# Performance work log

Hardware: AMD Instinct MI355X
Metric: run time of the kernel (lower is better)

Reference implementation:

```python
import jax, jax.numpy as jnp
import numpy as np

N, E, G = 50000, 800000, 64
IN, EDGE = 128, 16
HID, H = 32, 4
FHID, HF = 64, 4
OUT = 16
NEG_SLOPE = 0.2


def _segment_softmax(logits, seg, num):
    m = jax.ops.segment_max(logits, seg, num_segments=num)
    m = jnp.where(jnp.isfinite(m), m, 0.0)
    p = jnp.exp(logits - m[seg])
    s = jax.ops.segment_sum(p, seg, num_segments=num)
    return p / (s[seg] + 1e-16)


def gatv2(x, src, dst, eattr, Wl, bl, Wr, br, We, att, bias, concat):
    # PyG GATv2Conv with add_self_loops=True (edge_attr fill_value='mean')
    n = x.shape[0]
    heads, ch = att.shape
    ones = jnp.ones((src.shape[0],), x.dtype)
    cnt = jax.ops.segment_sum(ones, dst, num_segments=n)
    mean_attr = jax.ops.segment_sum(eattr, dst, num_segments=n) / jnp.maximum(cnt, 1.0)[:, None]
    loop = jnp.arange(n)
    s = jnp.concatenate([src, loop])
    d = jnp.concatenate([dst, loop])
    ea = jnp.concatenate([eattr, mean_attr], axis=0)
    xl = (x @ Wl + bl).reshape(n, heads, ch)   # lin_l (source)
    xr = (x @ Wr + br).reshape(n, heads, ch)   # lin_r (target)
    ee = (ea @ We).reshape(-1, heads, ch)      # lin_edge (no bias)
    z = jax.nn.leaky_relu(xl[s] + xr[d] + ee, NEG_SLOPE)  # [E+N, H, C]
    logits = jnp.einsum('ehc,hc->eh', z, att)
    alpha = _segment_softmax(logits, d, n)
    out = jax.ops.segment_sum(alpha[:, :, None] * xl[s], d, num_segments=n)  # [N, H, C]
    out = out.reshape(n, heads * ch) if concat else out.mean(axis=1)
    return out + bias


def _forward(x, edge_attr, src, dst, batch,
             Wl0, bl0, Wr0, br0, We0, att0, bo0,
             Wlh, blh, Wrh, brh, Weh, atth, boh,
             Wlf, blf, Wrf, brf, Wef, attf, bof,
             Wlin, blin):
    h1 = jax.nn.relu(gatv2(x, src, dst, edge_attr, Wl0, bl0, Wr0, br0, We0, att0, bo0, True))
    h2 = jax.nn.relu(gatv2(h1, src, dst, edge_attr, Wlh, blh, Wrh, brh, Weh, atth, boh, True))
    h3 = jax.nn.relu(gatv2(h2, src, dst, edge_attr, Wlf, blf, Wrf, brf, Wef, attf, bof, False))
    # global_mean_pool over graphs
    gsum = jax.ops.segment_sum(h3, batch, num_segments=G)
    gcnt = jax.ops.segment_sum(jnp.ones((h3.shape[0],), h3.dtype), batch, num_segments=G)
    g = gsum / jnp.maximum(gcnt, 1.0)[:, None]
    return g @ Wlin + blin  # final_dropout inactive in eval mode


def setup_inputs():
    key = jax.random.key(0)
    ks = jax.random.split(key, 20)
    def p(i, shape, fan_in):
        return jax.random.normal(ks[i], shape, jnp.float32) / np.sqrt(fan_in)
    z = lambda *s: jnp.zeros(s, jnp.float32)
    return {
        'x': jax.random.normal(ks[0], (N, IN), jnp.float32),
        'edge_index': jax.random.randint(ks[1], (2, E), 0, N),
        'batch': jnp.sort(jax.random.randint(ks[2], (N,), 0, G)),
        'edge_attr': jax.random.normal(ks[3], (E, EDGE), jnp.float32),
        'Wl0': p(4, (IN, H * HID), IN), 'bl0': z(H * HID),
        'Wr0': p(5, (IN, H * HID), IN), 'br0': z(H * HID),
        'We0': p(6, (EDGE, H * HID), EDGE), 'att0': p(7, (H, HID), HID), 'bo0': z(H * HID),
        'Wlh': p(8, (H * HID, H * HID), H * HID), 'blh': z(H * HID),
        'Wrh': p(9, (H * HID, H * HID), H * HID), 'brh': z(H * HID),
        'Weh': p(10, (EDGE, H * HID), EDGE), 'atth': p(11, (H, HID), HID), 'boh': z(H * HID),
        'Wlf': p(12, (H * HID, HF * FHID), H * HID), 'blf': z(HF * FHID),
        'Wrf': p(13, (H * HID, HF * FHID), H * HID), 'brf': z(HF * FHID),
        'Wef': p(14, (EDGE, HF * FHID), EDGE), 'attf': p(15, (HF, FHID), FHID), 'bof': z(FHID),
        'Wlin': p(16, (FHID, OUT), FHID), 'blin': z(OUT),
    }


def reference(x, edge_index, batch, edge_attr, Wl0, bl0, Wr0, br0, We0, att0, bo0, Wlh, blh, Wrh, brh, Weh, atth, boh, Wlf, blf, Wrf, brf, Wef, attf, bof, Wlin, blin):
    return _forward(x, edge_attr, edge_index[0], edge_index[1], batch,
                    Wl0, bl0, Wr0, br0, We0, att0, bo0,
                    Wlh, blh, Wrh, brh, Weh, atth, boh,
                    Wlf, blf, Wrf, brf, Wef, attf, bof,
                    Wlin, blin)
```

## Files before the change

### kernel.cpp

```cpp
#include <hip/hip_runtime.h>
#include <cstddef>

#define NSLOPE 0.2f

constexpr int NN = 50000;
constexpr int EE = 800000;
constexpr int GG = 64;
constexpr int SCAN_B = 1024;

typedef unsigned short ushort_t;
typedef unsigned int uint_t;
typedef __bf16 bhalf;
typedef bhalf bhalf8 __attribute__((ext_vector_type(8)));
typedef float floatx4 __attribute__((ext_vector_type(4)));
typedef _Float16 half_t;
typedef half_t half2_t __attribute__((ext_vector_type(2)));

__device__ __forceinline__ ushort_t f2b(float f) {
  unsigned int u = __float_as_uint(f);
  unsigned int r = (u + 0x7fffu + ((u >> 16) & 1u)) >> 16;
  return (ushort_t)r;
}
__device__ __forceinline__ float b2f(ushort_t b) {
  return __uint_as_float(((unsigned int)b) << 16);
}
__device__ __forceinline__ uint_t packh2(float a, float b) {
  half2_t h = {(half_t)a, (half_t)b};
  return __builtin_bit_cast(uint_t, h);
}
__device__ __forceinline__ float dot2acc(uint_t ea, half2_t w, float c) {
  half2_t a = __builtin_bit_cast(half2_t, ea);
#if __has_builtin(__builtin_amdgcn_fdot2)
  return __builtin_amdgcn_fdot2(a, w, c, false);
#else
  return c + (float)a.x * (float)w.x + (float)a.y * (float)w.y;
#endif
}
__device__ __forceinline__ float fexp2(float x) {
#if __has_builtin(__builtin_amdgcn_exp2f)
  return __builtin_amdgcn_exp2f(x);
#else
  return exp2f(x);
#endif
}

__device__ __forceinline__ float red16(float x) {
  int v = __builtin_bit_cast(int, x);
  x += __builtin_bit_cast(float, __builtin_amdgcn_update_dpp(0, v, 0xB1, 0xF, 0xF, true));
  v = __builtin_bit_cast(int, x);
  x += __builtin_bit_cast(float, __builtin_amdgcn_update_dpp(0, v, 0x4E, 0xF, 0xF, true));
  v = __builtin_bit_cast(int, x);
  x += __builtin_bit_cast(float, __builtin_amdgcn_update_dpp(0, v, 0x124, 0xF, 0xF, true));
  v = __builtin_bit_cast(int, x);
  x += __builtin_bit_cast(float, __builtin_amdgcn_update_dpp(0, v, 0x128, 0xF, 0xF, true));
  return x;
}

__global__ void hist_kernel(const int* __restrict__ dst, int* __restrict__ hist, int E) {
  int e = blockIdx.x * blockDim.x + threadIdx.x;
  if (e < E) atomicAdd(&hist[dst[e]], 1);
}

__global__ void scan_block_kernel(const int* __restrict__ in, int* __restrict__ out,
                                  int* __restrict__ bsum, int n) {
  __shared__ int tmp[SCAN_B];
  int gid = blockIdx.x * SCAN_B + threadIdx.x;
  int v = (gid < n) ? in[gid] : 0;
  tmp[threadIdx.x] = v;
  __syncthreads();
  for (int off = 1; off < SCAN_B; off <<= 1) {
    int t = (threadIdx.x >= off) ? tmp[threadIdx.x - off] : 0;
    __syncthreads();
    tmp[threadIdx.x] += t;
    __syncthreads();
  }
  if (gid < n) out[gid] = tmp[threadIdx.x];
  if (threadIdx.x == SCAN_B - 1) bsum[blockIdx.x] = tmp[threadIdx.x];
}

__global__ void scan_totals_kernel(const int* __restrict__ bsum, int* __restrict__ boff, int nb) {
  if (blockIdx.x == 0 && threadIdx.x == 0) {
    int run = 0;
    for (int i = 0; i < nb; ++i) { boff[i] = run; run += bsum[i]; }
  }
}

__global__ void add_offsets_kernel(int* __restrict__ rowptr, const int* __restrict__ boff,
                                   int* __restrict__ cursor, int n) {
  int gid = blockIdx.x * SCAN_B + threadIdx.x;
  if (gid == 0) { rowptr[0] = 0; cursor[0] = 0; }
  if (gid < n) {
    int v = rowptr[1 + gid] + boff[blockIdx.x];
    rowptr[1 + gid] = v;
    if (1 + gid < n) cursor[1 + gid] = v;
  }
}

__global__ void scatter_fused_kernel(const int* __restrict__ dst, const int* __restrict__ src,
                                     const float* __restrict__ eattr, int* __restrict__ cursor,
                                     int* __restrict__ srcp, uint_t* __restrict__ eah, int E) {
  int e = blockIdx.x * blockDim.x + threadIdx.x;
  if (e >= E) return;
  const float4* a = reinterpret_cast<const float4*>(eattr + (size_t)e * 16);
  float4 f0 = a[0], f1 = a[1], f2 = a[2], f3 = a[3];
  int pos = atomicAdd(&cursor[dst[e]], 1);
  srcp[pos] = src[e];
  uint4 o0 = make_uint4(packh2(f0.x, f0.y), packh2(f0.z, f0.w),
                        packh2(f1.x, f1.y), packh2(f1.z, f1.w));
  uint4 o1 = make_uint4(packh2(f2.x, f2.y), packh2(f2.z, f2.w),
                        packh2(f3.x, f3.y), packh2(f3.z, f3.w));
  uint4* b = reinterpret_cast<uint4*>(eah + (size_t)pos * 8);
  b[0] = o0; b[1] = o1;
}

__global__ __launch_bounds__(256) void mean_attr_kernel(
    const int* __restrict__ rowptr, const uint_t* __restrict__ eah,
    uint_t* __restrict__ meanattr_h, int N) {
  const int lane = threadIdx.x & 63;
  int d = blockIdx.x * (blockDim.x >> 6) + (threadIdx.x >> 6);
  if (d >= N) return;
  int beg = rowptr[d], end = rowptr[d + 1];
  int k2 = lane & 7;
  int sub = lane >> 3;
  float ax = 0.f, ay = 0.f;
  for (int j = beg + sub; j < end; j += 8) {
    half2_t h = __builtin_bit_cast(half2_t, eah[(size_t)j * 8 + k2]);
    ax += (float)h.x; ay += (float)h.y;
  }
  ax += __shfl_xor(ax, 8);  ay += __shfl_xor(ay, 8);
  ax += __shfl_xor(ax, 16); ay += __shfl_xor(ay, 16);
  ax += __shfl_xor(ax, 32); ay += __shfl_xor(ay, 32);
  if (sub == 0) {
    int c = end - beg; if (c < 1) c = 1;
    float inv = 1.f / (float)c;
    meanattr_h[(size_t)d * 8 + k2] = packh2(ax * inv, ay * inv);
  }
}

__global__ void prep_w_kernel(const float* W0, ushort_t* T0, int n0,
                              const float* W1, ushort_t* T1, int n1,
                              const float* W2, ushort_t* T2, int n2,
                              const float* W3, ushort_t* T3, int n3,
                              const float* W4, ushort_t* T4, int n4,
                              const float* W5, ushort_t* T5, int n5) {
  const float* W; ushort_t* T; int Nc;
  switch (blockIdx.y) {
    case 0: W = W0; T = T0; Nc = n0; break;
    case 1: W = W1; T = T1; Nc = n1; break;
    case 2: W = W2; T = T2; Nc = n2; break;
    case 3: W = W3; T = T3; Nc = n3; break;
    case 4: W = W4; T = T4; Nc = n4; break;
    default: W = W5; T = T5; Nc = n5; break;
  }
  int idx = blockIdx.x * blockDim.x + threadIdx.x;
  if (idx >= Nc * 128) return;
  int n = idx >> 7, k = idx & 127;
  T[idx] = f2b(W[(size_t)k * Nc + n]);
}

__global__ void prep_we_kernel(const float* We0, const float* att0, uint_t* w0, float* a0,
                               const float* We1, const float* att1, uint_t* w1, float* a1,
                               const float* We2, const float* att2, uint_t* w2, float* a2) {
  const float* We; const float* att; uint_t* wp; float* ap; int C;
  switch (blockIdx.y) {
    case 0: We = We0; att = att0; wp = w0; ap = a0; C = 128; break;
    case 1: We = We1; att = att1; wp = w1; ap = a1; C = 128; break;
    default: We = We2; att = att2; wp = w2; ap = a2; C = 256; break;
  }
  int idx = blockIdx.x * blockDim.x + threadIdx.x;
  if (idx >= 9 * C) return;
  if (idx < 8 * C) {
    int sh = (C == 256) ? 8 : 7;
    int k2 = idx >> sh, ch = idx & (C - 1);
    wp[idx] = packh2(We[(size_t)(2 * k2) * C + ch], We[(size_t)(2 * k2 + 1) * C + ch]);
  } else {
    int ch = idx - 8 * C;
    ap[ch] = att[ch] * 1.44269504f;
  }
}

template <typename TA>
__global__ __launch_bounds__(256) void gemm_bt_dual_bf16(
    const TA* __restrict__ Xb,
    const ushort_t* __restrict__ Wt0, const float* __restrict__ b0, ushort_t* __restrict__ Y0,
    const ushort_t* __restrict__ Wt1, const float* __restrict__ b1, ushort_t* __restrict__ Y1,
    int M, int Nc) {
  constexpr int K = 128, BM = 128, LDT = 136;
  __shared__ ushort_t Als[BM * LDT];
  __shared__ ushort_t Bls[BM * LDT];
  int nb = Nc >> 7;
  int half = blockIdx.y / nb;
  int cb = blockIdx.y % nb;
  const ushort_t* Wt = half ? Wt1 : Wt0;
  const float* bias = half ? b1 : b0;
  ushort_t* Y = half ? Y1 : Y0;
  int r0 = blockIdx.x * BM;
  int col0 = cb * 128;
  int tid = threadIdx.x;
  {
    int rl = tid >> 5;
    int kq = (tid & 31) * 4;
#pragma unroll
    for (int s = 0; s < 16; ++s) {
      int row = rl + s * 8;
      int grow = r0 + row;
      ushort4 v = make_ushort4(0, 0, 0, 0);
      if (grow < M) {
        if constexpr (sizeof(TA) == 4) {
          float4 f = *reinterpret_cast<const float4*>(Xb + (size_t)grow * K + kq);
          v = make_ushort4(f2b(f.x), f2b(f.y), f2b(f.z), f2b(f.w));
        } else {
          v = *reinterpret_cast<const ushort4*>(Xb + (size_t)grow * K + kq);
        }
      }
      *reinterpret_cast<ushort4*>(&Als[row * LDT + kq]) = v;
      ushort4 wv = *reinterpret_cast<const ushort4*>(Wt + (size_t)(col0 + row) * K + kq);
      *reinterpret_cast<ushort4*>(&Bls[row * LDT + kq]) = wv;
    }
  }
  __syncthreads();
  int lane = tid & 63;
  int w = tid >> 6;
  int m0 = (w >> 1) * 64;
  int n0 = (w & 1) * 64;
  int rin = lane & 15, quad = lane >> 4;
  floatx4 acc[4][4];
#pragma unroll
  for (int i = 0; i < 4; ++i)
#pragma unroll
    for (int j = 0; j < 4; ++j) acc[i][j] = (floatx4){0.f, 0.f, 0.f, 0.f};
#pragma unroll
  for (int kt = 0; kt < 4; ++kt) {
    int ko = kt * 32 + quad * 8;
    bhalf8 af[4], bf[4];
#pragma unroll
    for (int i = 0; i < 4; ++i)
      af[i] = *reinterpret_cast<const bhalf8*>(&Als[(m0 + i * 16 + rin) * LDT + ko]);
#pragma unroll
    for (int i = 0; i < 4; ++i)
      bf[i] = *reinterpret_cast<const bhalf8*>(&Bls[(n0 + i * 16 + rin) * LDT + ko]);
#pragma unroll
    for (int mi = 0; mi < 4; ++mi)
#pragma unroll
      for (int ni = 0; ni < 4; ++ni)
        acc[mi][ni] = __builtin_amdgcn_mfma_f32_16x16x32_bf16(af[mi], bf[ni], acc[mi][ni], 0, 0, 0);
  }
#pragma unroll
  for (int ni = 0; ni < 4; ++ni) {
    int gcol = col0 + n0 + ni * 16 + rin;
    float bb = bias[gcol];
#pragma unroll
    for (int mi = 0; mi < 4; ++mi) {
      int growb = r0 + m0 + mi * 16 + quad * 4;
#pragma unroll
      for (int r = 0; r < 4; ++r) {
        int grow = growb + r;
        if (grow < M) Y[(size_t)grow * Nc + gcol] = f2b(acc[mi][ni][r] + bb);
      }
    }
  }
}

template <int VPL>
__device__ __forceinline__ void loadb(const ushort_t* p, float* v) {
  if constexpr (VPL == 2) {
    ushort2 t = *reinterpret_cast<const ushort2*>(p);
    v[0] = b2f(t.x); v[1] = b2f(t.y);
  } else {
    ushort4 t = *reinterpret_cast<const ushort4*>(p);
    v[0] = b2f(t.x); v[1] = b2f(t.y); v[2] = b2f(t.z); v[3] = b2f(t.w);
  }
}
template <int VPL>
__device__ __forceinline__ void storeb(ushort_t* p, const float* v) {
  if constexpr (VPL == 2) {
    *reinterpret_cast<ushort2*>(p) = make_ushort2(f2b(v[0]), f2b(v[1]));
  } else {
    *reinterpret_cast<ushort4*>(p) = make_ushort4(f2b(v[0]), f2b(v[1]), f2b(v[2]), f2b(v[3]));
  }
}

template <int VPL>
__device__ __forceinline__ float lrelu_dot(const float* xv, const float* rv,
                                           const half2_t (*wepk)[VPL], const float* areg,
                                           const uint_t* ea) {
  float part = 0.f;
#pragma unroll
  for (int j = 0; j < VPL; ++j) {
    float z = xv[j] + rv[j];
#pragma unroll
    for (int k2 = 0; k2 < 8; ++k2) z = dot2acc(ea[k2], wepk[k2][j], z);
    float zl = fmaxf(z, NSLOPE * z);
    part = fmaf(zl, areg[j], part);
  }
  return red16(part);
}

template <int EB, int VPL, int C>
__device__ __forceinline__ void process_group(
    const int* __restrict__ srcp, const uint_t* __restrict__ eah, int j,
    const ushort_t* __restrict__ xl, int lane, const float* rv,
    const half2_t (*wepk)[VPL], const float* areg,
    float& s, float* acc) {
  int sn[EB];
#pragma unroll
  for (int u = 0; u < EB; ++u) sn[u] = srcp[j + u];
  float xv[EB][VPL];
#pragma unroll
  for (int u = 0; u < EB; ++u) loadb<VPL>(xl + (size_t)sn[u] * C + lane * VPL, xv[u]);
  float lg[EB];
#pragma unroll
  for (int u = 0; u < EB; ++u) {
    const uint4* ap4 = reinterpret_cast<const uint4*>(eah + (size_t)(j + u) * 8);
    uint4 e0 = ap4[0], e1 = ap4[1];
    uint_t ea[8] = {e0.x, e0.y, e0.z, e0.w, e1.x, e1.y, e1.z, e1.w};
    lg[u] = lrelu_dot<VPL>(xv[u], rv, wepk, areg, ea);
  }
  float p[EB], ps = 0.f;
#pragma unroll
  for (int u = 0; u < EB; ++u) { p[u] = fexp2(lg[u]); ps += p[u]; }
  s += ps;
#pragma unroll
  for (int jj = 0; jj < VPL; ++jj) {
    float t = p[0] * xv[0][jj];
#pragma unroll
    for (int u = 1; u < EB; ++u) t = fmaf(p[u], xv[u][jj], t);
    acc[jj] += t;
  }
}

template <int VPL, int C>
__device__ __forceinline__ void process_edge(
    int sn, const uint_t* ea,
    const ushort_t* __restrict__ xl, int lane, const float* rv,
    const half2_t (*wepk)[VPL], const float* areg,
    float& s, float* acc) {
  float xv[VPL];
  loadb<VPL>(xl + (size_t)sn * C + lane * VPL, xv);
  float lg = lrelu_dot<VPL>(xv, rv, wepk, areg, ea);
  float p = fexp2(lg);
  s += p;
#pragma unroll
  for (int jj = 0; jj < VPL; ++jj) acc[jj] = fmaf(p, xv[jj], acc[jj]);
}

template <int C, bool FINAL>
__global__ __launch_bounds__(128) void gat_fused_kernel(
    const int* __restrict__ rowptr,
    const int* __restrict__ srcp, const uint_t* __restrict__ eah,
    const uint_t* __restrict__ meanattr_h,
    const ushort_t* __restrict__ xl, const ushort_t* __restrict__ xr,
    const uint_t* __restrict__ wep,
    const float* __restrict__ atts,
    const float* __restrict__ bias, ushort_t* __restrict__ hout, int N) {
  constexpr int VPL = C / 64;
  const int lane = threadIdx.x & 63;
  int d = __builtin_amdgcn_readfirstlane(blockIdx.x * 2 + (threadIdx.x >> 6));
  if (d >= N) return;

  half2_t wepk[8][VPL];
  float areg[VPL];
#pragma unroll
  for (int k2 = 0; k2 < 8; ++k2)
#pragma unroll
    for (int jj = 0; jj < VPL; ++jj)
      wepk[k2][jj] = __builtin_bit_cast(half2_t, wep[k2 * C + lane * VPL + jj]);
#pragma unroll
  for (int jj = 0; jj < VPL; ++jj) areg[jj] = atts[lane * VPL + jj];

  int beg = rowptr[d], end = rowptr[d + 1];
  float rv[VPL];
  loadb<VPL>(xr + (size_t)d * C + lane * VPL, rv);

  float s = 0.f;
  float acc[VPL];
#pragma unroll
  for (int jj = 0; jj < VPL; ++jj) acc[jj] = 0.f;

  int j = beg;
  if constexpr (C == 128) {
    for (; j + 8 <= end; j += 8)
      process_group<8, VPL, C>(srcp, eah, j, xl, lane, rv, wepk, areg, s, acc);
  }
  for (; j + 4 <= end; j += 4)
    process_group<4, VPL, C>(srcp, eah, j, xl, lane, rv, wepk, areg, s, acc);
  for (; j + 2 <= end; j += 2)
    process_group<2, VPL, C>(srcp, eah, j, xl, lane, rv, wepk, areg, s, acc);
  for (; j < end; ++j)
    process_group<1, VPL, C>(srcp, eah, j, xl, lane, rv, wepk, areg, s, acc);

  {
    const uint4* mp4 = reinterpret_cast<const uint4*>(meanattr_h + (size_t)d * 8);
    uint4 e0 = mp4[0], e1 = mp4[1];
    uint_t ea[8] = {e0.x, e0.y, e0.z, e0.w, e1.x, e1.y, e1.z, e1.w};
    process_edge<VPL, C>(d, ea, xl, lane, rv, wepk, areg, s, acc);
  }

  float inv = 1.f / (s + 1e-16f);
  if constexpr (!FINAL) {
    float res[VPL];
#pragma unroll
    for (int jj = 0; jj < VPL; ++jj) {
      float v = acc[jj] * inv + bias[lane * VPL + jj];
      res[jj] = v > 0.f ? v : 0.f;
    }
    storeb<VPL>(hout + (size_t)d * C + lane * VPL, res);
  } else {
    float v[VPL];
#pragma unroll
    for (int jj = 0; jj < VPL; ++jj) v[jj] = acc[jj] * inv;
#pragma unroll
    for (int jj = 0; jj < VPL; ++jj) {
      v[jj] += __shfl_xor(v[jj], 16);
      v[jj] += __shfl_xor(v[jj], 32);
    }
    if (lane < 16) {
      float res[VPL];
#pragma unroll
      for (int jj = 0; jj < VPL; ++jj) {
        float val = 0.25f * v[jj] + bias[lane * VPL + jj];
        res[jj] = val > 0.f ? val : 0.f;
      }
      storeb<VPL>(hout + (size_t)d * 64 + lane * VPL, res);
    }
  }
}

__global__ __launch_bounds__(256) void pool_kernel(
    const ushort_t* __restrict__ h3, const int* __restrict__ batch,
    float* __restrict__ gsum, float* __restrict__ gcnt, int N) {
  const int lane = threadIdx.x & 63;
  const int w = blockIdx.x * (blockDim.x >> 6) + (threadIdx.x >> 6);
  const int nw = gridDim.x * (blockDim.x >> 6);
  const int chunk = (N + nw - 1) / nw;
  int i0 = w * chunk;
  int i1 = i0 + chunk; if (i1 > N) i1 = N;
  if (i0 >= i1) return;
  int cur = batch[i0];
  float acc = 0.f;
  int cnt = 0;
  for (int i = i0; i < i1; ++i) {
    int g = batch[i];
    if (g != cur) {
      atomicAdd(&gsum[(size_t)cur * 64 + lane], acc);
      if (lane == 0) atomicAdd(&gcnt[cur], (float)cnt);
      acc = 0.f; cnt = 0; cur = g;
    }
    acc += b2f(h3[(size_t)i * 64 + lane]);
    ++cnt;
  }
  atomicAdd(&gsum[(size_t)cur * 64 + lane], acc);
  if (lane == 0) atomicAdd(&gcnt[cur], (float)cnt);
}

__global__ void final_kernel(const float* __restrict__ gsum, const float* __restrict__ gcnt,
                             const float* __restrict__ Wlin, const float* __restrict__ blin,
                             float* __restrict__ out) {
  int idx = blockIdx.x * blockDim.x + threadIdx.x;
  if (idx >= GG * 16) return;
  int g = idx >> 4, o = idx & 15;
  float c = gcnt[g];
  c = c > 1.f ? c : 1.f;
  float inv = 1.f / c;
  float acc = blin[o];
  for (int f = 0; f < 64; ++f) acc = fmaf(gsum[(size_t)g * 64 + f] * inv, Wlin[f * 16 + o], acc);
  out[idx] = acc;
}

extern "C" void kernel_launch(void* const* d_in, const int* in_sizes, int n_in,
                              void* d_out, int out_size, void* d_ws, size_t ws_size,
                              hipStream_t stream) {
  (void)in_sizes; (void)n_in; (void)out_size; (void)ws_size;
  const float* x     = (const float*)d_in[0];
  const int*   eidx  = (const int*)d_in[1];
  const int*   batch = (const int*)d_in[2];
  const float* eattr = (const float*)d_in[3];
  const float* Wl0 = (const float*)d_in[4];  const float* bl0 = (const float*)d_in[5];
  const float* Wr0 = (const float*)d_in[6];  const float* br0 = (const float*)d_in[7];
  const float* We0 = (const float*)d_in[8];  const float* att0 = (const float*)d_in[9];
  const float* bo0 = (const float*)d_in[10];
  const float* Wlh = (const float*)d_in[11]; const float* blh = (const float*)d_in[12];
  const float* Wrh = (const float*)d_in[13]; const float* brh = (const float*)d_in[14];
  const float* Weh = (const float*)d_in[15]; const float* atth = (const float*)d_in[16];
  const float* boh = (const float*)d_in[17];
  const float* Wlf = (const float*)d_in[18]; const float* blf = (const float*)d_in[19];
  const float* Wrf = (const float*)d_in[20]; const float* brf = (const float*)d_in[21];
  const float* Wef = (const float*)d_in[22]; const float* attf = (const float*)d_in[23];
  const float* bof = (const float*)d_in[24];
  const float* Wlin = (const float*)d_in[25]; const float* blin = (const float*)d_in[26];

  const int* src = eidx;
  const int* dst = eidx + EE;

  char* ws = (char*)d_ws;
  size_t off = 0;
  auto take = [&](size_t bytes) -> void* {
    void* p = ws + off;
    off += (bytes + 1023) & ~(size_t)1023;
    return p;
  };
  ushort_t* xl     = (ushort_t*)take((size_t)NN * 256 * 2);
  ushort_t* xr     = (ushort_t*)take((size_t)NN * 256 * 2);
  ushort_t* hb     = (ushort_t*)take((size_t)NN * 128 * 2);
  uint_t* meanattr_h = (uint_t*)take((size_t)NN * 8 * 4);
  int* hist        = (int*)take((size_t)NN * 4);
  float* gsum      = (float*)take((size_t)GG * 64 * 4);
  float* gcnt      = (float*)take((size_t)GG * 4);
  int* rowptr      = (int*)take((size_t)(NN + 1) * 4);
  int* cursor      = (int*)take((size_t)NN * 4);
  int* bsum        = (int*)take(256);
  int* boff        = (int*)take(256);
  ushort_t* wtl0   = (ushort_t*)take((size_t)128 * 128 * 2);
  ushort_t* wtr0   = (ushort_t*)take((size_t)128 * 128 * 2);
  ushort_t* wtlh   = (ushort_t*)take((size_t)128 * 128 * 2);
  ushort_t* wtrh   = (ushort_t*)take((size_t)128 * 128 * 2);
  ushort_t* wtlf   = (ushort_t*)take((size_t)256 * 128 * 2);
  ushort_t* wtrf   = (ushort_t*)take((size_t)256 * 128 * 2);
  int* srcp        = (int*)take((size_t)EE * 4);
  uint_t* eah      = (uint_t*)take((size_t)EE * 8 * 4);
  uint_t* we0p     = (uint_t*)take((size_t)8 * 128 * 4);
  uint_t* wehp     = (uint_t*)take((size_t)8 * 128 * 4);
  uint_t* wefp     = (uint_t*)take((size_t)8 * 256 * 4);
  float* att0s     = (float*)take((size_t)128 * 4);
  float* atths     = (float*)take((size_t)128 * 4);
  float* attfs     = (float*)take((size_t)256 * 4);

  hipMemsetAsync(hist, 0, 200704 + 16384 + 256, stream);
  hist_kernel<<<(EE + 255) / 256, 256, 0, stream>>>(dst, hist, EE);
  int nsb = (NN + SCAN_B - 1) / SCAN_B;
  scan_block_kernel<<<nsb, SCAN_B, 0, stream>>>(hist, rowptr + 1, bsum, NN);
  scan_totals_kernel<<<1, 64, 0, stream>>>(bsum, boff, nsb);
  add_offsets_kernel<<<nsb, SCAN_B, 0, stream>>>(rowptr, boff, cursor, NN);
  scatter_fused_kernel<<<(EE + 255) / 256, 256, 0, stream>>>(dst, src, eattr, cursor, srcp, eah, EE);
  mean_attr_kernel<<<(NN + 3) / 4, 256, 0, stream>>>(rowptr, eah, meanattr_h, NN);
  prep_w_kernel<<<dim3(128, 6), 256, 0, stream>>>(Wl0, wtl0, 128, Wr0, wtr0, 128,
                                                  Wlh, wtlh, 128, Wrh, wtrh, 128,
                                                  Wlf, wtlf, 256, Wrf, wtrf, 256);
  prep_we_kernel<<<dim3(9, 3), 256, 0, stream>>>(We0, att0, we0p, att0s,
                                                 Weh, atth, wehp, atths,
                                                 Wef, attf, wefp, attfs);

  const int GEMM_MB = (NN + 127) / 128;
  const int GAT_BLOCKS = (NN + 1) / 2;

  gemm_bt_dual_bf16<float><<<dim3(GEMM_MB, 2), 256, 0, stream>>>(
      x, wtl0, bl0, xl, wtr0, br0, xr, NN, 128);
  gat_fused_kernel<128, false><<<GAT_BLOCKS, 128, 0, stream>>>(
      rowptr, srcp, eah, meanattr_h, xl, xr, we0p, att0s, bo0, hb, NN);
  gemm_bt_dual_bf16<ushort_t><<<dim3(GEMM_MB, 2), 256, 0, stream>>>(
      hb, wtlh, blh, xl, wtrh, brh, xr, NN, 128);
  gat_fused_kernel<128, false><<<GAT_BLOCKS, 128, 0, stream>>>(
      rowptr, srcp, eah, meanattr_h, xl, xr, wehp, atths, boh, hb, NN);
  gemm_bt_dual_bf16<ushort_t><<<dim3(GEMM_MB, 4), 256, 0, stream>>>(
      hb, wtlf, blf, xl, wtrf, brf, xr, NN, 256);
  gat_fused_kernel<256, true><<<GAT_BLOCKS, 128, 0, stream>>>(
      rowptr, srcp, eah, meanattr_h, xl, xr, wefp, attfs, bof, hb, NN);
  pool_kernel<<<128, 256, 0, stream>>>(hb, batch, gsum, gcnt, NN);
  final_kernel<<<4, 256, 0, stream>>>(gsum, gcnt, Wlin, blin, (float*)d_out);
}
```

Before: 672.7 us.

## Reuse GEMM input tile across both projections, persistent GAT blocks, warp scan

The dual GEMM now loads the A tile once and loops over the left and right weight matrices, so the input is read and converted only once per block instead of once per projection. The GAT kernel becomes a grid-stride persistent kernel with 4096 blocks, so edge weights, attention vectors and bias are loaded once per wave and reused across many nodes instead of reloaded per node. The block-total scan becomes a wavefront shuffle scan instead of a single-thread serial loop. In exchange there are fewer GEMM blocks and a serialized inner loop over the two projections, and the persistent GAT has a static node-to-wave assignment that may load-balance worse on skewed degrees.

```diff
diff --git a/kernel.cpp b/kernel.cpp
--- a/kernel.cpp
+++ b/kernel.cpp
@@ -79,10 +79,14 @@
 }
 
 __global__ void scan_totals_kernel(const int* __restrict__ bsum, int* __restrict__ boff, int nb) {
-  if (blockIdx.x == 0 && threadIdx.x == 0) {
-    int run = 0;
-    for (int i = 0; i < nb; ++i) { boff[i] = run; run += bsum[i]; }
-  }
+  int lane = threadIdx.x;
+  int orig = (lane < nb) ? bsum[lane] : 0;
+  int v = orig;
+  for (int off = 1; off < 64; off <<= 1) {
+    int t = __shfl_up(v, off);
+    if (lane >= off) v += t;
+  }
+  if (lane < nb) boff[lane] = v - orig;
 }
 
 __global__ void add_offsets_kernel(int* __restrict__ rowptr, const int* __restrict__ boff,
@@ -188,74 +192,77 @@
   constexpr int K = 128, BM = 128, LDT = 136;
   __shared__ ushort_t Als[BM * LDT];
   __shared__ ushort_t Bls[BM * LDT];
-  int nb = Nc >> 7;
-  int half = blockIdx.y / nb;
-  int cb = blockIdx.y % nb;
-  const ushort_t* Wt = half ? Wt1 : Wt0;
-  const float* bias = half ? b1 : b0;
-  ushort_t* Y = half ? Y1 : Y0;
   int r0 = blockIdx.x * BM;
-  int col0 = cb * 128;
+  int col0 = blockIdx.y * 128;
   int tid = threadIdx.x;
-  {
-    int rl = tid >> 5;
-    int kq = (tid & 31) * 4;
-#pragma unroll
-    for (int s = 0; s < 16; ++s) {
-      int row = rl + s * 8;
-      int grow = r0 + row;
-      ushort4 v = make_ushort4(0, 0, 0, 0);
-      if (grow < M) {
-        if constexpr (sizeof(TA) == 4) {
-          float4 f = *reinterpret_cast<const float4*>(Xb + (size_t)grow * K + kq);
-          v = make_ushort4(f2b(f.x), f2b(f.y), f2b(f.z), f2b(f.w));
-        } else {
-          v = *reinterpret_cast<const ushort4*>(Xb + (size_t)grow * K + kq);
-        }
+  int rl = tid >> 5;
+  int kq = (tid & 31) * 4;
+#pragma unroll
+  for (int s = 0; s < 16; ++s) {
+    int row = rl + s * 8;
+    int grow = r0 + row;
+    ushort4 v = make_ushort4(0, 0, 0, 0);
+    if (grow < M) {
+      if constexpr (sizeof(TA) == 4) {
+        float4 f = *reinterpret_cast<const float4*>(Xb + (size_t)grow * K + kq);
+        v = make_ushort4(f2b(f.x), f2b(f.y), f2b(f.z), f2b(f.w));
+      } else {
+        v = *reinterpret_cast<const ushort4*>(Xb + (size_t)grow * K + kq);
       }
-      *reinterpret_cast<ushort4*>(&Als[row * LDT + kq]) = v;
-      ushort4 wv = *reinterpret_cast<const ushort4*>(Wt + (size_t)(col0 + row) * K + kq);
-      *reinterpret_cast<ushort4*>(&Bls[row * LDT + kq]) = wv;
-    }
-  }
-  __syncthreads();
+    }
+    *reinterpret_cast<ushort4*>(&Als[row * LDT + kq]) = v;
+  }
   int lane = tid & 63;
   int w = tid >> 6;
   int m0 = (w >> 1) * 64;
   int n0 = (w & 1) * 64;
   int rin = lane & 15, quad = lane >> 4;
-  floatx4 acc[4][4];
-#pragma unroll
-  for (int i = 0; i < 4; ++i)
-#pragma unroll
-    for (int j = 0; j < 4; ++j) acc[i][j] = (floatx4){0.f, 0.f, 0.f, 0.f};
-#pragma unroll
-  for (int kt = 0; kt < 4; ++kt) {
-    int ko = kt * 32 + quad * 8;
-    bhalf8 af[4], bf[4];
+
+  for (int half = 0; half < 2; ++half) {
+    const ushort_t* Wt = half ? Wt1 : Wt0;
+    const float* bias = half ? b1 : b0;
+    ushort_t* Y = half ? Y1 : Y0;
+    __syncthreads();
+#pragma unroll
+    for (int s = 0; s < 16; ++s) {
+      int row = rl + s * 8;
+      ushort4 wv = *reinterpret_cast<const ushort4*>(Wt + (size_t)(col0 + row) * K + kq);
+      *reinterpret_cast<ushort4*>(&Bls[row * LDT + kq]) = wv;
+    }
+    __syncthreads();
+    floatx4 acc[4][4];
 #pragma unroll
     for (int i = 0; i < 4; ++i)
-      af[i] = *reinterpret_cast<const bhalf8*>(&Als[(m0 + i * 16 + rin) * LDT + ko]);
-#pragma unroll
-    for (int i = 0; i < 4; ++i)
-      bf[i] = *reinterpret_cast<const bhalf8*>(&Bls[(n0 + i * 16 + rin) * LDT + ko]);
-#pragma unroll
-    for (int mi = 0; mi < 4; ++mi)
-#pragma unroll
-      for (int ni = 0; ni < 4; ++ni)
-        acc[mi][ni] = __builtin_amdgcn_mfma_f32_16x16x32_bf16(af[mi], bf[ni], acc[mi][ni], 0, 0, 0);
-  }
-#pragma unroll
-  for (int ni = 0; ni < 4; ++ni) {
-    int gcol = col0 + n0 + ni * 16 + rin;
-    float bb = bias[gcol];
-#pragma unroll
-    for (int mi = 0; mi < 4; ++mi) {
-      int growb = r0 + m0 + mi * 16 + quad * 4;
-#pragma unroll
-      for (int r = 0; r < 4; ++r) {
-        int grow = growb + r;
-        if (grow < M) Y[(size_t)grow * Nc + gcol] = f2b(acc[mi][ni][r] + bb);
+#pragma unroll
+      for (int j = 0; j < 4; ++j) acc[i][j] = (floatx4){0.f, 0.f, 0.f, 0.f};
+#pragma unroll
+    for (int kt = 0; kt < 4; ++kt) {
+      int ko = kt * 32 + quad * 8;
+      bhalf8 af[4], bf[4];
+#pragma unroll
+      for (int i = 0; i < 4; ++i)
+        af[i] = *reinterpret_cast<const bhalf8*>(&Als[(m0 + i * 16 + rin) * LDT + ko]);
+#pragma unroll
+      for (int i = 0; i < 4; ++i)
+        bf[i] = *reinterpret_cast<const bhalf8*>(&Bls[(n0 + i * 16 + rin) * LDT + ko]);
+#pragma unroll
+      for (int mi = 0; mi < 4; ++mi)
+#pragma unroll
+        for (int ni = 0; ni < 4; ++ni)
+          acc[mi][ni] = __builtin_amdgcn_mfma_f32_16x16x32_bf16(af[mi], bf[ni], acc[mi][ni], 0, 0, 0);
+    }
+#pragma unroll
+    for (int ni = 0; ni < 4; ++ni) {
+      int gcol = col0 + n0 + ni * 16 + rin;
+      float bb = bias[gcol];
+#pragma unroll
+      for (int mi = 0; mi < 4; ++mi) {
+        int growb = r0 + m0 + mi * 16 + quad * 4;
+#pragma unroll
+        for (int r = 0; r < 4; ++r) {
+          int grow = growb + r;
+          if (grow < M) Y[(size_t)grow * Nc + gcol] = f2b(acc[mi][ni][r] + bb);
+        }
       }
     }
   }
@@ -355,11 +362,11 @@
     const float* __restrict__ bias, ushort_t* __restrict__ hout, int N) {
   constexpr int VPL = C / 64;
   const int lane = threadIdx.x & 63;
-  int d = __builtin_amdgcn_readfirstlane(blockIdx.x * 2 + (threadIdx.x >> 6));
-  if (d >= N) return;
+  const int w0 = blockIdx.x * 2 + (threadIdx.x >> 6);
+  const int nw = gridDim.x * 2;
 
   half2_t wepk[8][VPL];
-  float areg[VPL];
+  float areg[VPL], breg[VPL];
 #pragma unroll
   for (int k2 = 0; k2 < 8; ++k2)
 #pragma unroll
@@ -367,61 +374,67 @@
       wepk[k2][jj] = __builtin_bit_cast(half2_t, wep[k2 * C + lane * VPL + jj]);
 #pragma unroll
   for (int jj = 0; jj < VPL; ++jj) areg[jj] = atts[lane * VPL + jj];
-
-  int beg = rowptr[d], end = rowptr[d + 1];
-  float rv[VPL];
-  loadb<VPL>(xr + (size_t)d * C + lane * VPL, rv);
-
-  float s = 0.f;
-  float acc[VPL];
-#pragma unroll
-  for (int jj = 0; jj < VPL; ++jj) acc[jj] = 0.f;
-
-  int j = beg;
-  if constexpr (C == 128) {
-    for (; j + 8 <= end; j += 8)
-      process_group<8, VPL, C>(srcp, eah, j, xl, lane, rv, wepk, areg, s, acc);
-  }
-  for (; j + 4 <= end; j += 4)
-    process_group<4, VPL, C>(srcp, eah, j, xl, lane, rv, wepk, areg, s, acc);
-  for (; j + 2 <= end; j += 2)
-    process_group<2, VPL, C>(srcp, eah, j, xl, lane, rv, wepk, areg, s, acc);
-  for (; j < end; ++j)
-    process_group<1, VPL, C>(srcp, eah, j, xl, lane, rv, wepk, areg, s, acc);
-
-  {
-    const uint4* mp4 = reinterpret_cast<const uint4*>(meanattr_h + (size_t)d * 8);
-    uint4 e0 = mp4[0], e1 = mp4[1];
-    uint_t ea[8] = {e0.x, e0.y, e0.z, e0.w, e1.x, e1.y, e1.z, e1.w};
-    process_edge<VPL, C>(d, ea, xl, lane, rv, wepk, areg, s, acc);
-  }
-
-  float inv = 1.f / (s + 1e-16f);
-  if constexpr (!FINAL) {
-    float res[VPL];
-#pragma unroll
-    for (int jj = 0; jj < VPL; ++jj) {
-      float v = acc[jj] * inv + bias[lane * VPL + jj];
-      res[jj] = v > 0.f ? v : 0.f;
-    }
-    storeb<VPL>(hout + (size_t)d * C + lane * VPL, res);
-  } else {
-    float v[VPL];
-#pragma unroll
-    for (int jj = 0; jj < VPL; ++jj) v[jj] = acc[jj] * inv;
-#pragma unroll
-    for (int jj = 0; jj < VPL; ++jj) {
-      v[jj] += __shfl_xor(v[jj], 16);
-      v[jj] += __shfl_xor(v[jj], 32);
-    }
-    if (lane < 16) {
+#pragma unroll
+  for (int jj = 0; jj < VPL; ++jj)
+    breg[jj] = (!FINAL || lane < 16) ? bias[lane * VPL + jj] : 0.f;
+
+  for (int dd = w0; dd < N; dd += nw) {
+    int d = __builtin_amdgcn_readfirstlane(dd);
+    int beg = rowptr[d], end = rowptr[d + 1];
+    float rv[VPL];
+    loadb<VPL>(xr + (size_t)d * C + lane * VPL, rv);
+
+    float s = 0.f;
+    float acc[VPL];
+#pragma unroll
+    for (int jj = 0; jj < VPL; ++jj) acc[jj] = 0.f;
+
+    int j = beg;
+    if constexpr (C == 128) {
+      for (; j + 8 <= end; j += 8)
+        process_group<8, VPL, C>(srcp, eah, j, xl, lane, rv, wepk, areg, s, acc);
+    }
+    for (; j + 4 <= end; j += 4)
+      process_group<4, VPL, C>(srcp, eah, j, xl, lane, rv, wepk, areg, s, acc);
+    for (; j + 2 <= end; j += 2)
+      process_group<2, VPL, C>(srcp, eah, j, xl, lane, rv, wepk, areg, s, acc);
+    for (; j < end; ++j)
+      process_group<1, VPL, C>(srcp, eah, j, xl, lane, rv, wepk, areg, s, acc);
+
+    {
+      const uint4* mp4 = reinterpret_cast<const uint4*>(meanattr_h + (size_t)d * 8);
+      uint4 e0 = mp4[0], e1 = mp4[1];
+      uint_t ea[8] = {e0.x, e0.y, e0.z, e0.w, e1.x, e1.y, e1.z, e1.w};
+      process_edge<VPL, C>(d, ea, xl, lane, rv, wepk, areg, s, acc);
+    }
+
+    float inv = 1.f / (s + 1e-16f);
+    if constexpr (!FINAL) {
       float res[VPL];
 #pragma unroll
       for (int jj = 0; jj < VPL; ++jj) {
-        float val = 0.25f * v[jj] + bias[lane * VPL + jj];
-        res[jj] = val > 0.f ? val : 0.f;
+        float v = acc[jj] * inv + breg[jj];
+        res[jj] = v > 0.f ? v : 0.f;
       }
-      storeb<VPL>(hout + (size_t)d * 64 + lane * VPL, res);
+      storeb<VPL>(hout + (size_t)d * C + lane * VPL, res);
+    } else {
+      float v[VPL];
+#pragma unroll
+      for (int jj = 0; jj < VPL; ++jj) v[jj] = acc[jj] * inv;
+#pragma unroll
+      for (int jj = 0; jj < VPL; ++jj) {
+        v[jj] += __shfl_xor(v[jj], 16);
+        v[jj] += __shfl_xor(v[jj], 32);
+      }
+      if (lane < 16) {
+        float res[VPL];
+#pragma unroll
+        for (int jj = 0; jj < VPL; ++jj) {
+          float val = 0.25f * v[jj] + breg[jj];
+          res[jj] = val > 0.f ? val : 0.f;
+        }
+        storeb<VPL>(hout + (size_t)d * 64 + lane * VPL, res);
+      }
     }
   }
 }
@@ -541,19 +554,19 @@
                                                  Wef, attf, wefp, attfs);
 
   const int GEMM_MB = (NN + 127) / 128;
-  const int GAT_BLOCKS = (NN + 1) / 2;
-
-  gemm_bt_dual_bf16<float><<<dim3(GEMM_MB, 2), 256, 0, stream>>>(
+  const int GAT_PBLK = 4096;
+
+  gemm_bt_dual_bf16<float><<<dim3(GEMM_MB, 1), 256, 0, stream>>>(
       x, wtl0, bl0, xl, wtr0, br0, xr, NN, 128);
-  gat_fused_kernel<128, false><<<GAT_BLOCKS, 128, 0, stream>>>(
+  gat_fused_kernel<128, false><<<GAT_PBLK, 128, 0, stream>>>(
       rowptr, srcp, eah, meanattr_h, xl, xr, we0p, att0s, bo0, hb, NN);
+  gemm_bt_dual_bf16<ushort_t><<<dim3(GEMM_MB, 1), 256, 0, stream>>>(
+      hb, wtlh, blh, xl, wtrh, brh, xr, NN, 128);
+  gat_fused_kernel<128, false><<<GAT_PBLK, 128, 0, stream>>>(
+      rowptr, srcp, eah, meanattr_h, xl, xr, wehp, atths, boh, hb, NN);
   gemm_bt_dual_bf16<ushort_t><<<dim3(GEMM_MB, 2), 256, 0, stream>>>(
-      hb, wtlh, blh, xl, wtrh, brh, xr, NN, 128);
-  gat_fused_kernel<128, false><<<GAT_BLOCKS, 128, 0, stream>>>(
-      rowptr, srcp, eah, meanattr_h, xl, xr, wehp, atths, boh, hb, NN);
-  gemm_bt_dual_bf16<ushort_t><<<dim3(GEMM_MB, 4), 256, 0, stream>>>(
       hb, wtlf, blf, xl, wtrf, brf, xr, NN, 256);
-  gat_fused_kernel<256, true><<<GAT_BLOCKS, 128, 0, stream>>>(
+  gat_fused_kernel<256, true><<<GAT_PBLK, 128, 0, stream>>>(
       rowptr, srcp, eah, meanattr_h, xl, xr, wefp, attfs, bof, hb, NN);
   pool_kernel<<<128, 256, 0, stream>>>(hb, batch, gsum, gcnt, NN);
   final_kernel<<<4, 256, 0, stream>>>(gsum, gcnt, Wlin, blin, (float*)d_out);
```

Result: slower. 694.6 us (+3.3%).
